# Performance work log

Measured on AMD Instinct MI355X. Metric: run time of the kernel, lower is better.

Reference implementation:

```python
import jax, jax.numpy as jnp
import numpy as np

N_HEAD = 16

def setup_inputs() -> dict:
    key = jax.random.key(0)
    ks = jax.random.split(key, 5)
    B, T, C = 8, 1024, 1024
    s = 0.02
    return {
        "x": jax.random.normal(ks[0], (B, T, C), jnp.float32),
        "W_qkv": jax.random.normal(ks[1], (C, 3 * C), jnp.float32) * s,
        "b_qkv": jnp.zeros((3 * C,), jnp.float32),
        "W_proj": jax.random.normal(ks[2], (C, C), jnp.float32) * s,
        "b_proj": jnp.zeros((C,), jnp.float32),
    }

def reference(x, W_qkv, b_qkv, W_proj, b_proj):
    B, T, C = x.shape
    H = N_HEAD
    hs = C // H
    qkv = x @ W_qkv + b_qkv                       # [B,T,3C]
    q, k, v = jnp.split(qkv, 3, axis=-1)
    # [B,T,C] -> [B,H,T,hs]
    q = q.reshape(B, T, H, hs).transpose(0, 2, 1, 3)
    k = k.reshape(B, T, H, hs).transpose(0, 2, 1, 3)
    v = v.reshape(B, T, H, hs).transpose(0, 2, 1, 3)
    scores = jnp.einsum('bhqd,bhkd->bhqk', q, k) * (hs ** -0.5)  # [B,H,T,T]
    causal = jnp.tril(jnp.ones((T, T), dtype=bool))
    scores = jnp.where(causal[None, None], scores, jnp.finfo(scores.dtype).min)
    attn = jax.nn.softmax(scores, axis=-1)
    # dropout layers are identity in eval mode
    out = jnp.einsum('bhqk,bhkd->bhqd', attn, v)  # [B,H,T,hs]
    out = out.transpose(0, 2, 1, 3).reshape(B, T, C)
    return out @ W_proj + b_proj
```

## Files before the change

### kernel.cpp

```cpp
#include <hip/hip_runtime.h>

#define TT 1024
#define CC 1024
#define NH 16
#define HS 64

typedef __attribute__((ext_vector_type(8))) short short8;
typedef __attribute__((ext_vector_type(4))) float f32x4;

__device__ inline unsigned short f2bf(float f) {
  unsigned int u = __float_as_uint(f);
  unsigned int r = u + 0x7FFFu + ((u >> 16) & 1u);
  return (unsigned short)(r >> 16);
}

__device__ inline unsigned int cvtpk_bf16(float lo, float hi) {
  unsigned int r;
  asm("v_cvt_pk_bf16_f32 %0, %1, %2" : "=v"(r) : "v"(lo), "v"(hi));
  return r;
}

#define GLDS16(g, l)                                                         \
  __builtin_amdgcn_global_load_lds(                                          \
      (const __attribute__((address_space(1))) void*)(g),                    \
      (__attribute__((address_space(3))) void*)(l), 16, 0, 0)

__global__ __launch_bounds__(256) void f32_to_bf16(
    const float* __restrict__ in, unsigned short* __restrict__ out, int n4) {
  int i = (blockIdx.x * 256 + threadIdx.x);
  if (i >= n4) return;
  float4 v = *(const float4*)&in[(size_t)i * 4];
  ushort4 o;
  o.x = f2bf(v.x); o.y = f2bf(v.y); o.z = f2bf(v.z); o.w = f2bf(v.w);
  *(ushort4*)&out[(size_t)i * 4] = o;
}

__global__ __launch_bounds__(256) void transpose_to_bf16(
    const float* __restrict__ W, unsigned short* __restrict__ Wt,
    int K, int N) {
  __shared__ float tile[32][33];
  const int n0 = blockIdx.x * 32, k0 = blockIdx.y * 32;
  const int t = threadIdx.x;
  {
    const int kr = t >> 3;
    const int nc = (t & 7) * 4;
    float4 v = *(const float4*)&W[(size_t)(k0 + kr) * N + n0 + nc];
    tile[kr][nc + 0] = v.x; tile[kr][nc + 1] = v.y;
    tile[kr][nc + 2] = v.z; tile[kr][nc + 3] = v.w;
  }
  __syncthreads();
  {
    const int nr = t >> 3;
    const int kc = (t & 7) * 4;
    ushort4 o;
    o.x = f2bf(tile[kc + 0][nr]);
    o.y = f2bf(tile[kc + 1][nr]);
    o.z = f2bf(tile[kc + 2][nr]);
    o.w = f2bf(tile[kc + 3][nr]);
    *(ushort4*)&Wt[(size_t)(n0 + nr) * K + k0 + kc] = o;
  }
}

template <bool BF16_OUT>
__global__ __launch_bounds__(512, 4) void gemm_bt_256(
    const unsigned short* __restrict__ A,
    const unsigned short* __restrict__ Bt,
    const float* __restrict__ bias,
    void* __restrict__ Cv,
    int M, int N, int K) {
  __shared__ __attribute__((aligned(16))) unsigned short As[2][256 * 32];
  __shared__ __attribute__((aligned(16))) unsigned short Bs[2][128 * 32];

  const int tid = threadIdx.x;
  const int w = tid >> 6, l = tid & 63;
  const int lr = l & 15, lg = l >> 4;
  const int wr = w >> 1, wc = w & 1;

  const int gx = gridDim.x;
  const int nwg = gx * gridDim.y;
  int f = blockIdx.y * gx + blockIdx.x;
  f = (f & 7) * (nwg >> 3) + (f >> 3);
  const int bx = f % gx, by = f / gx;
  const int brow = by * 256, bcol = bx * 128;

  const int ga0 = tid, ga1 = 512 + tid;
  const int ar0 = ga0 >> 2, ac0 = ga0 & 3;
  const int ar1 = ga1 >> 2, ac1 = ga1 & 3;
  const int br_ = tid >> 2, bc_ = tid & 3;
  const unsigned short* Asrc0 =
      A + (size_t)(brow + ar0) * K + (ac0 ^ ((ar0 >> 1) & 3)) * 8;
  const unsigned short* Asrc1 =
      A + (size_t)(brow + ar1) * K + (ac1 ^ ((ar1 >> 1) & 3)) * 8;
  const unsigned short* Bsrc =
      Bt + (size_t)(bcol + br_) * K + (bc_ ^ ((br_ >> 1) & 3)) * 8;

  typedef __attribute__((address_space(3))) unsigned short lds_us;

#define STAGE(bb, kt)                                                        \
  do {                                                                       \
    const int k0_ = (kt) * 32;                                               \
    GLDS16(Asrc0 + k0_, (lds_us*)&As[bb][0] + ga0 * 8);                      \
    GLDS16(Asrc1 + k0_, (lds_us*)&As[bb][0] + ga1 * 8);                      \
    GLDS16(Bsrc + k0_, (lds_us*)&Bs[bb][0] + tid * 8);                       \
  } while (0)

  f32x4 acc[4][4] = {};

  const int sfr = ((((lr >> 1) & 3) ^ lg) * 8);
  const int arow0 = wr * 64 + lr;
  const int brow0 = wc * 64 + lr;

#define KSTEP(cur, kt, VMASM, DOSTAGE)                                       \
  do {                                                                       \
    asm volatile(VMASM ::: "memory");                                        \
    __builtin_amdgcn_sched_barrier(0);                                       \
    __builtin_amdgcn_s_barrier();     \
    short8 af[4], bf[4];                                                     \
    _Pragma("unroll") for (int mi_ = 0; mi_ < 4; ++mi_)                      \
        af[mi_] = *(const short8*)&As[cur][(arow0 + mi_ * 16) * 32 + sfr];   \
    _Pragma("unroll") for (int ni_ = 0; ni_ < 4; ++ni_)                      \
        bf[ni_] = *(const short8*)&Bs[cur][(brow0 + ni_ * 16) * 32 + sfr];   \
    asm volatile("s_waitcnt lgkmcnt(0)" ::: "memory");                       \
    __builtin_amdgcn_sched_barrier(0);                                       \
    __builtin_amdgcn_s_barrier();          \
    __builtin_amdgcn_sched_barrier(0);                                       \
    if (DOSTAGE) STAGE(cur, (kt) + 2);                                       \
    __builtin_amdgcn_s_setprio(1);                                           \
    _Pragma("unroll") for (int mi_ = 0; mi_ < 4; ++mi_)                      \
        _Pragma("unroll") for (int ni_ = 0; ni_ < 4; ++ni_)                  \
            acc[mi_][ni_] = __builtin_amdgcn_mfma_f32_16x16x32_bf16(         \
                af[mi_], bf[ni_], acc[mi_][ni_], 0, 0, 0);                   \
    __builtin_amdgcn_s_setprio(0);                                           \
  } while (0)

  const int nk = K >> 5;
  STAGE(0, 0);
  STAGE(1, 1);
  int cur = 0;
  for (int t = 0; t < nk - 1; ++t) {
    KSTEP(cur, t, "s_waitcnt vmcnt(3)", (t + 2 < nk));
    cur ^= 1;
  }
  KSTEP(cur, nk - 1, "s_waitcnt vmcnt(0)", false);
#undef KSTEP
#undef STAGE

#pragma unroll
  for (int ni = 0; ni < 4; ++ni) {
    const int col = bcol + wc * 64 + ni * 16 + lr;
    const float bv = bias[col];
#pragma unroll
    for (int mi = 0; mi < 4; ++mi) {
      const int row0 = brow + wr * 64 + mi * 16 + lg * 4;
#pragma unroll
      for (int j = 0; j < 4; ++j) {
        const float val = acc[mi][ni][j] + bv;
        if (BF16_OUT)
          ((unsigned short*)Cv)[(size_t)(row0 + j) * N + col] = f2bf(val);
        else
          ((float*)Cv)[(size_t)(row0 + j) * N + col] = val;
      }
    }
  }
}

#define C1 0.18033688f

__global__ __launch_bounds__(256) void attn_mfma(
    const unsigned short* __restrict__ qkv, unsigned short* __restrict__ aout) {
  const int bh = blockIdx.y;
  const int b = bh >> 4, h = bh & 15;
  const int tid = threadIdx.x;
  const int w = tid >> 6;
  const int l = tid & 63;
  const int lr = l & 15;
  const int lg = l >> 4;

  __shared__ __attribute__((aligned(16))) unsigned short Kl[64 * 64];
  __shared__ __attribute__((aligned(16))) unsigned short Vt[64 * 64];
  __shared__ __attribute__((aligned(16))) unsigned short Pq[4][32 * 64];

  const size_t row3c = 3 * CC;
  const unsigned short* qbase = qkv + (size_t)(b * TT) * row3c + h * HS;
  const unsigned short* kbase = qbase + CC;
  const unsigned short* vbase = qbase + 2 * CC;

  const int ksrow = 16 * w + (l >> 3);
  const int ksbyte = (((l & 7) ^ (l >> 3)) << 4);
  typedef __attribute__((address_space(3))) unsigned short lds_us;
  lds_us* KlW0 = (lds_us*)Kl + (16 * w) * 64;
  lds_us* KlW1 = (lds_us*)Kl + (16 * w + 8) * 64;

#pragma unroll 1
  for (int pass = 0; pass < 2; ++pass) {
    const int qt = pass ? (7 - blockIdx.x) : blockIdx.x;
    const int qw = qt * 128 + w * 32;

    short8 aq[2][2];
#pragma unroll
    for (int mi = 0; mi < 2; ++mi)
#pragma unroll
      for (int ks = 0; ks < 2; ++ks)
        aq[mi][ks] = *(const short8*)(qbase +
            (size_t)(qw + mi * 16 + lr) * row3c + ks * 32 + lg * 8);

    f32x4 sOT[4][2] = {};
    float lpart[2] = {0.f, 0.f};

    const int ntiles = 2 * qt + 2;
    for (int kt = 0; kt < ntiles; ++kt) {
      const int k0 = kt * 64;
      GLDS16((const char*)(kbase + (size_t)(k0 + ksrow) * row3c) + ksbyte, KlW0);
      GLDS16((const char*)(kbase + (size_t)(k0 + 8 + ksrow) * row3c) + ksbyte, KlW1);
      {
        const unsigned short* vsrc = vbase + (size_t)(k0 + l) * row3c + 16 * w;
        short8 v0 = *(const short8*)(vsrc);
        short8 v1 = *(const short8*)(vsrc + 8);
#pragma unroll
        for (int i = 0; i < 8; ++i) {
          const int d0 = 16 * w + i, d1 = d0 + 8;
          Vt[(d0 * 64 + l) ^ ((d0 & 7) << 3)] = (unsigned short)v0[i];
          Vt[(d1 * 64 + l) ^ ((d1 & 7) << 3)] = (unsigned short)v1[i];
        }
      }
      __syncthreads();

      if (k0 <= qw + 31) {
        f32x4 sacc[4][2] = {};
        short8 ak[4][2];
#pragma unroll
        for (int ni = 0; ni < 4; ++ni) {
          const int tok = ni * 16 + lr;
          const int sw = (tok & 7) << 3;
#pragma unroll
          for (int ks = 0; ks < 2; ++ks)
            ak[ni][ks] = *(const short8*)&Kl[tok * 64 + ((ks * 32 + lg * 8) ^ sw)];
        }
#pragma unroll
        for (int ni = 0; ni < 4; ++ni)
#pragma unroll
          for (int mi = 0; mi < 2; ++mi)
#pragma unroll
            for (int ks = 0; ks < 2; ++ks)
              sacc[ni][mi] = __builtin_amdgcn_mfma_f32_16x16x32_bf16(
                  ak[ni][ks], aq[mi][ks], sacc[ni][mi], 0, 0, 0);

        const bool diag = (k0 + 63 > qw);
#pragma unroll
        for (int mi = 0; mi < 2; ++mi) {
          const int qloc = mi * 16 + lr;
          const int qglob = qw + qloc;
          const int psw = (qloc & 7) << 3;
          float ls = 0.f;
#pragma unroll
          for (int ni = 0; ni < 4; ++ni) {
            float p[4];
#pragma unroll
            for (int jj = 0; jj < 4; ++jj) {
              const float pv = exp2f(fmaf(sacc[ni][mi][jj], C1, -2.0f));
              const int kvg = k0 + ni * 16 + lg * 4 + jj;
              p[jj] = (diag && (kvg > qglob)) ? 0.f : pv;
            }
            ls += (p[0] + p[1]) + (p[2] + p[3]);
            uint2 pk;
            pk.x = cvtpk_bf16(p[0], p[1]);
            pk.y = cvtpk_bf16(p[2], p[3]);
            *(uint2*)&Pq[w][qloc * 64 + ((ni * 16 + lg * 4) ^ psw)] = pk;
          }
          lpart[mi] += ls;
        }

        short8 av[4][2], bp[2][2];
#pragma unroll
        for (int nd = 0; nd < 4; ++nd) {
          const int d = nd * 16 + lr;
          const int sw = (d & 7) << 3;
#pragma unroll
          for (int ks = 0; ks < 2; ++ks)
            av[nd][ks] = *(const short8*)&Vt[d * 64 + ((ks * 32 + lg * 8) ^ sw)];
        }
#pragma unroll
        for (int mi = 0; mi < 2; ++mi) {
          const int qloc = mi * 16 + lr;
          const int psw = (qloc & 7) << 3;
#pragma unroll
          for (int ks = 0; ks < 2; ++ks)
            bp[mi][ks] = *(const short8*)&Pq[w][qloc * 64 + ((ks * 32 + lg * 8) ^ psw)];
        }
#pragma unroll
        for (int nd = 0; nd < 4; ++nd)
#pragma unroll
          for (int mi = 0; mi < 2; ++mi)
#pragma unroll
            for (int ks = 0; ks < 2; ++ks)
              sOT[nd][mi] = __builtin_amdgcn_mfma_f32_16x16x32_bf16(
                  av[nd][ks], bp[mi][ks], sOT[nd][mi], 0, 0, 0);
      }
      __syncthreads();
    }

#pragma unroll
    for (int mi = 0; mi < 2; ++mi) {
      float ls = lpart[mi];
      ls += __shfl_xor(ls, 16);
      ls += __shfl_xor(ls, 32);
      const float inv = 1.f / ls;
      const size_t row = (size_t)(b * TT + qw + mi * 16 + lr);
#pragma unroll
      for (int nd = 0; nd < 4; ++nd) {
        uint2 pk;
        pk.x = cvtpk_bf16(sOT[nd][mi][0] * inv, sOT[nd][mi][1] * inv);
        pk.y = cvtpk_bf16(sOT[nd][mi][2] * inv, sOT[nd][mi][3] * inv);
        *(uint2*)&aout[row * CC + h * HS + nd * 16 + lg * 4] = pk;
      }
    }
  }
}

extern "C" void kernel_launch(void* const* d_in, const int* in_sizes, int n_in,
                              void* d_out, int out_size, void* d_ws, size_t ws_size,
                              hipStream_t stream) {
  const float* x     = (const float*)d_in[0];
  const float* Wqkv  = (const float*)d_in[1];
  const float* bqkv  = (const float*)d_in[2];
  const float* Wproj = (const float*)d_in[3];
  const float* bproj = (const float*)d_in[4];
  float* out = (float*)d_out;

  char* ws = (char*)d_ws;
  unsigned short* qkvb   = (unsigned short*)ws;
  unsigned short* xb     = (unsigned short*)(ws + 50331648);
  unsigned short* attnb  = (unsigned short*)(ws + 67108864);
  unsigned short* wqkvt  = (unsigned short*)(ws + 83886080);
  unsigned short* wprojt = (unsigned short*)(ws + 90177536);

  const int M = 8 * TT;

  f32_to_bf16<<<dim3(8192), dim3(256), 0, stream>>>(x, xb, M * CC / 4);
  transpose_to_bf16<<<dim3(96, 32), dim3(256), 0, stream>>>(Wqkv, wqkvt, CC, 3 * CC);
  transpose_to_bf16<<<dim3(32, 32), dim3(256), 0, stream>>>(Wproj, wprojt, CC, CC);

  gemm_bt_256<true><<<dim3(3 * CC / 128, M / 256), dim3(512), 0, stream>>>(
      xb, wqkvt, bqkv, qkvb, M, 3 * CC, CC);

  attn_mfma<<<dim3(4, 8 * NH), dim3(256), 0, stream>>>(qkvb, attnb);

  gemm_bt_256<false><<<dim3(CC / 128, M / 256), dim3(512), 0, stream>>>(
      attnb, wprojt, bproj, out, M, CC, CC);
}
```

Baseline: 244.1 us.

## Use 256x256-tile 8-phase pipelined GEMM for QKV projection

Adds a new GEMM kernel with 256x256 output tiles, K-step 64, and 128KB of dynamic LDS. It interleaves LDS fragment loads, MFMA quarters and staggered global-to-LDS staging of the next tiles across barrier-separated phases. The QKV projection now uses this kernel instead of the 256x128 one, to raise data reuse per tile and overlap memory with compute. The cost is lower occupancy (two blocks per CU by launch bounds, one in practice with 128KB LDS), more accumulator registers, and fewer workgroups (384) to fill the CUs.

Result: slower. 251.7 us (+3.1%).

```diff
diff --git a/kernel.cpp b/kernel.cpp
--- a/kernel.cpp
+++ b/kernel.cpp
@@ -62,6 +62,132 @@
 }
 
 template <bool BF16_OUT>
+__global__ __launch_bounds__(512, 2) void gemm_8ph(
+    const unsigned short* __restrict__ A,
+    const unsigned short* __restrict__ Bt,
+    const float* __restrict__ bias,
+    void* __restrict__ Cv,
+    int M, int N, int K) {
+  extern __shared__ __attribute__((aligned(16))) unsigned short smg[];
+  typedef __attribute__((address_space(3))) unsigned short lds_us;
+  lds_us* sml = (lds_us*)smg;
+
+  const int tid = threadIdx.x;
+  const int w = tid >> 6, l = tid & 63;
+  const int lr = l & 15, lg = l >> 4;
+  const int wm = w >> 2, wn = w & 3;
+
+  const int gx = gridDim.x;
+  const int nwg = gx * gridDim.y;
+  int f = blockIdx.y * gx + blockIdx.x;
+  f = (f & 7) * (nwg >> 3) + (f >> 3);
+  const int bx = f % gx, by = f / gx;
+  const int brow = by * 256, bcol = bx * 256;
+
+  const int r0 = w * 8 + (l >> 3);
+  const int cs = (l & 7) ^ (l >> 3);
+  const unsigned short* Asrc = A + (size_t)(brow + r0) * K + cs * 8;
+  const unsigned short* Bsrc = Bt + (size_t)(bcol + r0) * K + cs * 8;
+  const int wlds = w * 512;
+
+#define ST_A(dd, hh, qq, kt)                                                 \
+  GLDS16(Asrc + (size_t)((hh)*128 + (qq)*64) * K + (kt) * 64,                \
+         sml + (dd)*16384 + (hh)*8192 + (qq)*4096 + wlds)
+#define ST_B(dd, hh, qq, kt)                                                 \
+  GLDS16(Bsrc + (size_t)((hh)*128 + (qq)*64) * K + (kt) * 64,                \
+         sml + 32768 + (dd)*16384 + (hh)*8192 + (qq)*4096 + wlds)
+
+  f32x4 acc[8][4] = {};
+  short8 afA[4][2], bfB[4][2];
+
+  const int ck0 = ((lg) ^ (lr & 7)) * 8;
+  const int ck1 = ((4 | lg) ^ (lr & 7)) * 8;
+  const int abase = wm * 8192 + lr * 64;
+  const int bbase = 32768 + (wn >> 1) * 8192 + (wn & 1) * 4096 + lr * 64;
+
+#define LDA(MI0)                                                             \
+  _Pragma("unroll") for (int mi = 0; mi < 4; ++mi) {                         \
+    afA[mi][0] = *(const short8*)(smg + bb * 16384 + abase + ((MI0) + mi) * 1024 + ck0); \
+    afA[mi][1] = *(const short8*)(smg + bb * 16384 + abase + ((MI0) + mi) * 1024 + ck1); \
+  }
+#define LDB(NI0)                                                             \
+  _Pragma("unroll") for (int ni = 0; ni < 2; ++ni) {                         \
+    bfB[(NI0) + ni][0] = *(const short8*)(smg + bb * 16384 + bbase + ((NI0) + ni) * 1024 + ck0); \
+    bfB[(NI0) + ni][1] = *(const short8*)(smg + bb * 16384 + bbase + ((NI0) + ni) * 1024 + ck1); \
+  }
+#define MFMA_Q(MI0, NI0)                                                     \
+  __builtin_amdgcn_s_setprio(1);                                             \
+  _Pragma("unroll") for (int mi = 0; mi < 4; ++mi)                           \
+  _Pragma("unroll") for (int ni = 0; ni < 2; ++ni)                           \
+  _Pragma("unroll") for (int ks = 0; ks < 2; ++ks)                           \
+    acc[(MI0) + mi][(NI0) + ni] = __builtin_amdgcn_mfma_f32_16x16x32_bf16(   \
+        afA[mi][ks], bfB[(NI0) + ni][ks], acc[(MI0) + mi][(NI0) + ni], 0, 0, 0); \
+  __builtin_amdgcn_s_setprio(0);
+#define WAIT_LGKM                                                            \
+  asm volatile("s_waitcnt lgkmcnt(0)" ::: "memory");                         \
+  __builtin_amdgcn_sched_barrier(0);
+
+  const int nk = K >> 6;
+
+#pragma unroll
+  for (int tt = 0; tt < 2; ++tt) {
+    ST_A(tt, 0, 0, tt); ST_A(tt, 0, 1, tt); ST_A(tt, 1, 0, tt); ST_A(tt, 1, 1, tt);
+    ST_B(tt, 0, 0, tt); ST_B(tt, 0, 1, tt); ST_B(tt, 1, 0, tt); ST_B(tt, 1, 1, tt);
+  }
+
+  for (int t = 0; t < nk; ++t) {
+    const int bb = t & 1;
+    const bool dostage = (t + 2 < nk);
+    if (t == nk - 1) { asm volatile("s_waitcnt vmcnt(0)" ::: "memory"); }
+    else             { asm volatile("s_waitcnt vmcnt(8)" ::: "memory"); }
+    __builtin_amdgcn_sched_barrier(0);
+    __builtin_amdgcn_s_barrier();
+    LDA(0); LDB(0);
+    WAIT_LGKM;
+    MFMA_Q(0, 0);
+    __builtin_amdgcn_s_barrier();
+    LDB(2);
+    WAIT_LGKM;
+    MFMA_Q(0, 2);
+    __builtin_amdgcn_s_barrier();
+    if (dostage) { ST_B(bb, 0, 0, t + 2); ST_B(bb, 0, 1, t + 2);
+                   ST_B(bb, 1, 0, t + 2); ST_B(bb, 1, 1, t + 2); }
+    LDA(4);
+    WAIT_LGKM;
+    MFMA_Q(4, 0);
+    __builtin_amdgcn_s_barrier();
+    if (dostage) { ST_A(bb, 0, 0, t + 2); ST_A(bb, 0, 1, t + 2);
+                   ST_A(bb, 1, 0, t + 2); ST_A(bb, 1, 1, t + 2); }
+    MFMA_Q(4, 2);
+    __builtin_amdgcn_s_barrier();
+  }
+#undef ST_A
+#undef ST_B
+#undef LDA
+#undef LDB
+#undef MFMA_Q
+#undef WAIT_LGKM
+
+#pragma unroll
+  for (int ni = 0; ni < 4; ++ni) {
+    const int col = bcol + wn * 64 + ni * 16 + lr;
+    const float bv = bias[col];
+#pragma unroll
+    for (int mi = 0; mi < 8; ++mi) {
+      const int row0 = brow + wm * 128 + mi * 16 + lg * 4;
+#pragma unroll
+      for (int j = 0; j < 4; ++j) {
+        const float val = acc[mi][ni][j] + bv;
+        if (BF16_OUT)
+          ((unsigned short*)Cv)[(size_t)(row0 + j) * N + col] = f2bf(val);
+        else
+          ((float*)Cv)[(size_t)(row0 + j) * N + col] = val;
+      }
+    }
+  }
+}
+
+template <bool BF16_OUT>
 __global__ __launch_bounds__(512, 4) void gemm_bt_256(
     const unsigned short* __restrict__ A,
     const unsigned short* __restrict__ Bt,
@@ -114,7 +240,7 @@
   do {                                                                       \
     asm volatile(VMASM ::: "memory");                                        \
     __builtin_amdgcn_sched_barrier(0);                                       \
-    __builtin_amdgcn_s_barrier();     \
+    __builtin_amdgcn_s_barrier();                                            \
     short8 af[4], bf[4];                                                     \
     _Pragma("unroll") for (int mi_ = 0; mi_ < 4; ++mi_)                      \
         af[mi_] = *(const short8*)&As[cur][(arow0 + mi_ * 16) * 32 + sfr];   \
@@ -122,7 +248,7 @@
         bf[ni_] = *(const short8*)&Bs[cur][(brow0 + ni_ * 16) * 32 + sfr];   \
     asm volatile("s_waitcnt lgkmcnt(0)" ::: "memory");                       \
     __builtin_amdgcn_sched_barrier(0);                                       \
-    __builtin_amdgcn_s_barrier();          \
+    __builtin_amdgcn_s_barrier();                                            \
     __builtin_amdgcn_sched_barrier(0);                                       \
     if (DOSTAGE) STAGE(cur, (kt) + 2);                                       \
     __builtin_amdgcn_s_setprio(1);                                           \
@@ -336,11 +462,14 @@
 
   const int M = 8 * TT;
 
+  (void)hipFuncSetAttribute((const void*)&gemm_8ph<true>,
+      hipFuncAttributeMaxDynamicSharedMemorySize, 131072);
+
   f32_to_bf16<<<dim3(8192), dim3(256), 0, stream>>>(x, xb, M * CC / 4);
   transpose_to_bf16<<<dim3(96, 32), dim3(256), 0, stream>>>(Wqkv, wqkvt, CC, 3 * CC);
   transpose_to_bf16<<<dim3(32, 32), dim3(256), 0, stream>>>(Wproj, wprojt, CC, CC);
 
-  gemm_bt_256<true><<<dim3(3 * CC / 128, M / 256), dim3(512), 0, stream>>>(
+  gemm_8ph<true><<<dim3(3 * CC / 256, M / 256), dim3(512), 131072, stream>>>(
       xb, wqkvt, bqkv, qkvb, M, 3 * CC, CC);
 
   attn_mfma<<<dim3(4, 8 * NH), dim3(256), 0, stream>>>(qkvb, attnb);
```
